# Kernel optimization log

Hardware: AMD Instinct MI355X
Metric: run time of the kernel (lower is better)

Reference implementation:

```python
import jax, jax.numpy as jnp
import numpy as np

S, B, T = 512, 256, 128


def setup_inputs() -> dict:
    key = jax.random.key(0)
    k1, k2, k3, k4, k5, k6 = jax.random.split(key, 6)
    emissions = jax.random.normal(k1, (S, B, T), dtype=jnp.float32)
    # realistic monotone mask: each sequence has a random length in [1, S]
    lengths = jax.random.randint(k2, (B,), 1, S + 1)
    mask = (jnp.arange(S)[:, None] < lengths[None, :]).astype(jnp.float32)  # [S,B]
    tags = jax.random.randint(k3, (S, B), 0, T)
    transitions = jax.random.normal(k4, (T, T), dtype=jnp.float32)
    start_transitions = jax.random.normal(k5, (T,), dtype=jnp.float32)
    stop_transitions = jax.random.normal(k6, (T,), dtype=jnp.float32)
    return {
        "emissions": emissions,
        "mask": mask,
        "tags": tags,
        "transitions": transitions,
        "start_transitions": start_transitions,
        "stop_transitions": stop_transitions,
    }


def reference(emissions, mask, tags, transitions, start_transitions, stop_transitions):
    seq_len, batch, num_tags = emissions.shape

    # ---- log-partition (forward algorithm) + viterbi score, fused scan ----
    init = start_transitions + emissions[0]  # [B,T]

    def part_step(carry, xs):
        fv, vv = carry  # forward var, viterbi var: [B,T]
        em, m = xs      # em: [B,T], m: [B]
        # scores[b, j, k] = em[b, j] + transitions[j, k]  (j=next tag, k=prev tag)
        scores = em[:, :, None] + transitions[None, :, :]          # [B,T,T]
        lse = jax.nn.logsumexp(fv[:, None, :] + scores, axis=2)     # [B,T]
        vmax = jnp.max(vv[:, None, :] + scores, axis=2)             # [B,T]
        fv = m[:, None] * lse + (1.0 - m)[:, None] * fv
        vv = m[:, None] * vmax + (1.0 - m)[:, None] * vv
        return (fv, vv), None

    (fv, vv), _ = jax.lax.scan(part_step, (init, init), (emissions[1:], mask[1:]))
    total_score = jax.nn.logsumexp(fv + stop_transitions, axis=1)   # [B]
    best_path_score = jnp.max(vv + stop_transitions, axis=1)        # [B]

    # ---- gold path score ----
    barange = jnp.arange(batch)
    tag0 = tags[0]
    rps0 = start_transitions[tag0] + emissions[0, barange, tag0] * mask[0]

    def rp_step(carry, xs):
        rps, prev = carry
        cur, em, m = xs  # cur:[B] int, em:[B,T], m:[B]
        rps = rps + transitions[prev, cur] * m
        rps = rps + jnp.take_along_axis(em, cur[:, None], axis=1)[:, 0] * m
        prev = jnp.where(m == 1.0, cur, prev)
        return (rps, prev), None

    (rps, prev), _ = jax.lax.scan(rp_step, (rps0, tag0), (tags[1:], emissions[1:], mask[1:]))
    real_path_score = rps + stop_transitions[prev]

    loss = jnp.mean(total_score - real_path_score)
    return loss, real_path_score, total_score, best_path_score
```

## Files before the change

kernel.cpp:

```cpp
#include <hip/hip_runtime.h>
#include <math.h>

#define S_LEN 512
#define BATCH 256
#define NTAG  128
#define EMSTRIDE (BATCH * NTAG)

typedef float    f32x2 __attribute__((ext_vector_type(2)));
typedef float    f32x4 __attribute__((ext_vector_type(4)));
typedef int      i32x4 __attribute__((ext_vector_type(4)));
typedef _Float16 h16x2 __attribute__((ext_vector_type(2)));

#define DPP_XOR1(x) __int_as_float(__builtin_amdgcn_mov_dpp(__float_as_int(x), 0xB1, 0xF, 0xF, false))
#define DPP_XOR2(x) __int_as_float(__builtin_amdgcn_mov_dpp(__float_as_int(x), 0x4E, 0xF, 0xF, false))

__device__ __forceinline__ int pkmax(int a, int b) {
  int r; asm("v_pk_max_f16 %0, %1, %2" : "=v"(r) : "v"(a), "v"(b)); return r;
}
__device__ __forceinline__ int pkmul(int a, int b) {
  int r; asm("v_pk_mul_f16 %0, %1, %2" : "=v"(r) : "v"(a), "v"(b)); return r;
}
__device__ __forceinline__ float dot2(int e, int w, float c) {
  return __builtin_amdgcn_fdot2(__builtin_bit_cast(h16x2, e),
                                __builtin_bit_cast(h16x2, w), c, false);
}
__device__ __forceinline__ int packh(float a, float b) {
  return __builtin_bit_cast(int, __builtin_amdgcn_cvt_pkrtz(a, b));
}
__device__ __forceinline__ f32x2 unpackh(int p) {
  h16x2 h = __builtin_bit_cast(h16x2, p);
  f32x2 r; r[0] = (float)h[0]; r[1] = (float)h[1]; return r;
}
__device__ __forceinline__ int emidx(bool isR, int len, int i) {
  int s = isR ? (len - 2 - i) : (1 + i);
  return s < 0 ? 0 : (s > S_LEN - 1 ? S_LEN - 1 : s);
}

__global__ __launch_bounds__(256, 1)
void crf_chain_kernel(const float* __restrict__ emis,
                      const float* __restrict__ mask,
                      const int* __restrict__ tags,
                      const float* __restrict__ trans,
                      const float* __restrict__ startt,
                      const float* __restrict__ stopt,
                      float* __restrict__ ws,
                      int* __restrict__ ewbuf,
                      float* __restrict__ out)
{
  const int blk = blockIdx.x;
  const int tid = threadIdx.x;

  __shared__ __align__(16) int cbuf[4][2][64];
  __shared__ float red[16];

  if (blk >= BATCH) {
    const int b = blk - BATCH;
    float part = 0.f, lenp = 0.f;
#pragma unroll
    for (int rep = 0; rep < 2; ++rep) {
      int s = tid + rep * 256;
      float m  = mask[(size_t)s * BATCH + b];
      int  cur = tags[(size_t)s * BATCH + b];
      if (s == 0) {
        part += startt[cur] + emis[(size_t)b * NTAG + cur] * m;
      } else {
        int prev = tags[(size_t)(s - 1) * BATCH + b];
        part += m * (trans[(size_t)prev * NTAG + cur] +
                     emis[((size_t)s * BATCH + b) * NTAG + cur]);
      }
      lenp += m;
    }
#pragma unroll
    for (int d = 1; d <= 32; d <<= 1) {
      part += __shfl_xor(part, d);
      lenp += __shfl_xor(lenp, d);
    }
    const int lane = tid & 63, wid = tid >> 6;
    if (lane == 0) { red[wid] = part; red[8 + wid] = lenp; }
    __syncthreads();
    if (tid == 0) {
      float rps = (red[0] + red[1]) + (red[2] + red[3]);
      float lf  = (red[8] + red[9]) + (red[10] + red[11]);
      int len = (int)(lf + 0.5f);
      int pf  = tags[(size_t)(len - 1) * BATCH + b];
      out[1 + b] = rps + stopt[pf];
    }
    return;
  }

  const int  b    = blk;
  const int  role = tid >> 6;
  const int  l    = tid & 63;
  const bool isR  = (role & 1) != 0;
  const bool isV  = (role >= 2);

  float mv = 0.f;
#pragma unroll
  for (int r = 0; r < 8; ++r) mv += mask[(size_t)(l + 64 * r) * BATCH + b];
#pragma unroll
  for (int d = 1; d <= 32; d <<= 1) mv += __shfl_xor(mv, d);
  const int len = (int)(mv + 0.5f);

  const int sm  = (len - 1) >> 1;
  const int nst = len - 1 - sm;
  const int cnt = isR ? nst : sm;

  int EA[64], EB[64];
  if (!isR) {
    const f32x4* r0 = (const f32x4*)(trans + (size_t)(2 * l) * NTAG);
    const f32x4* r1 = (const f32x4*)(trans + (size_t)(2 * l + 1) * NTAG);
#pragma unroll
    for (int mm = 0; mm < 32; ++mm) {
      f32x4 x0 = r0[mm], x1 = r1[mm];
      EA[2 * mm]     = packh(__expf(x0[0]), __expf(x0[1]));
      EA[2 * mm + 1] = packh(__expf(x0[2]), __expf(x0[3]));
      EB[2 * mm]     = packh(__expf(x1[0]), __expf(x1[1]));
      EB[2 * mm + 1] = packh(__expf(x1[2]), __expf(x1[3]));
    }
  } else {
#pragma unroll
    for (int m = 0; m < 64; ++m) {
      f32x2 p0 = *(const f32x2*)(trans + (size_t)(2 * m) * NTAG + 2 * l);
      f32x2 p1 = *(const f32x2*)(trans + (size_t)(2 * m + 1) * NTAG + 2 * l);
      EA[m] = packh(__expf(p0[0]), __expf(p1[0]));
      EB[m] = packh(__expf(p0[1]), __expf(p1[1]));
    }
  }

  const float* ebm = emis + (size_t)b * NTAG + 2 * l;
  float iA, iB;
  if (!isR) {
    iA = startt[2 * l]     + ebm[0];
    iB = startt[2 * l + 1] + ebm[1];
  } else {
    float eA = 0.f, eB = 0.f;
    if (nst > 0) {
      f32x2 e = *(const f32x2*)(ebm + (size_t)(len - 1) * EMSTRIDE);
      eA = e[0]; eB = e[1];
    }
    iA = stopt[2 * l]     + eA;
    iB = stopt[2 * l + 1] + eB;
  }
  float uA = __expf(iA), uB = __expf(iB);
  float mx0 = fmaxf(uA, uB);
  mx0 = fmaxf(mx0, DPP_XOR1(mx0));
  mx0 = fmaxf(mx0, DPP_XOR2(mx0));
  mx0 = fmaxf(mx0, __shfl_xor(mx0, 4));
  mx0 = fmaxf(mx0, __shfl_xor(mx0, 8));
  mx0 = fmaxf(mx0, __shfl_xor(mx0, 16));
  mx0 = fmaxf(mx0, __shfl_xor(mx0, 32));
  unsigned eb0 = (__float_as_uint(mx0) >> 23) & 0xFF;
  int Ew = (int)eb0 - 127;
  float sc0 = __uint_as_float((unsigned)(254 - eb0) << 23);
  cbuf[role][0][l] = packh(uA * sc0, uB * sc0);
  asm volatile("s_waitcnt lgkmcnt(0)" ::: "memory");

  f32x2 e0 = *(const f32x2*)(ebm + (size_t)emidx(isR, len, 0) * EMSTRIDE);
  f32x2 e1 = *(const f32x2*)(ebm + (size_t)emidx(isR, len, 1) * EMSTRIDE);
  f32x2 e2 = *(const f32x2*)(ebm + (size_t)emidx(isR, len, 2) * EMSTRIDE);
  f32x2 e3 = *(const f32x2*)(ebm + (size_t)emidx(isR, len, 3) * EMSTRIDE);

  int fin = cnt & 1;

#define TMAX(QQ) pkmax(pkmax(QQ[0], QQ[1]), pkmax(QQ[2], QQ[3]))

#define DQ(QQ, MB)                                                            \
      a0 = dot2(EA[(MB)+0], QQ[0], a0); b0 = dot2(EB[(MB)+0], QQ[0], b0);     \
      a1 = dot2(EA[(MB)+1], QQ[1], a1); b1 = dot2(EB[(MB)+1], QQ[1], b1);     \
      a2 = dot2(EA[(MB)+2], QQ[2], a2); b2 = dot2(EB[(MB)+2], QQ[2], b2);     \
      a3 = dot2(EA[(MB)+3], QQ[3], a3); b3 = dot2(EB[(MB)+3], QQ[3], b3);

#define VQ(QQ, MB)                                                            \
      pA0 = pkmax(pA0, pkmul(EA[(MB)+0], QQ[0]));                             \
      pB0 = pkmax(pB0, pkmul(EB[(MB)+0], QQ[0]));                             \
      pA1 = pkmax(pA1, pkmul(EA[(MB)+1], QQ[1]));                             \
      pB1 = pkmax(pB1, pkmul(EB[(MB)+1], QQ[1]));                             \
      pA2 = pkmax(pA2, pkmul(EA[(MB)+2], QQ[2]));                             \
      pB2 = pkmax(pB2, pkmul(EB[(MB)+2], QQ[2]));                             \
      pA3 = pkmax(pA3, pkmul(EA[(MB)+3], QQ[3]));                             \
      pB3 = pkmax(pB3, pkmul(EB[(MB)+3], QQ[3]));

#define STEP(U, EV)                                                           \
  {                                                                           \
    const int i_ = gb + (U);                                                  \
    if (i_ >= cnt) goto epi;                                                  \
    const i32x4* rp_ = (const i32x4*)cbuf[role][(U) & 1];                     \
    i32x4 Q0 = rp_[0],  Q1 = rp_[1],  Q2 = rp_[2],  Q3 = rp_[3];              \
    i32x4 Q4 = rp_[4],  Q5 = rp_[5],  Q6 = rp_[6],  Q7 = rp_[7];              \
    i32x4 Q8 = rp_[8],  Q9 = rp_[9],  Q10 = rp_[10], Q11 = rp_[11];           \
    i32x4 Q12 = rp_[12], Q13 = rp_[13], Q14 = rp_[14], Q15 = rp_[15];         \
    int t0 = TMAX(Q0),  t1 = TMAX(Q1),  t2 = TMAX(Q2),  t3 = TMAX(Q3);        \
    int t4 = TMAX(Q4),  t5 = TMAX(Q5),  t6 = TMAX(Q6),  t7 = TMAX(Q7);        \
    int t8 = TMAX(Q8),  t9 = TMAX(Q9),  t10 = TMAX(Q10), t11 = TMAX(Q11);     \
    int t12 = TMAX(Q12), t13 = TMAX(Q13), t14 = TMAX(Q14), t15 = TMAX(Q15);   \
    t0 = pkmax(t0, t1);   t2 = pkmax(t2, t3);                                 \
    t4 = pkmax(t4, t5);   t6 = pkmax(t6, t7);                                 \
    t8 = pkmax(t8, t9);   t10 = pkmax(t10, t11);                              \
    t12 = pkmax(t12, t13); t14 = pkmax(t14, t15);                             \
    t0 = pkmax(t0, t2); t4 = pkmax(t4, t6);                                   \
    t8 = pkmax(t8, t10); t12 = pkmax(t12, t14);                               \
    t0 = pkmax(t0, t4); t8 = pkmax(t8, t12); t0 = pkmax(t0, t8);              \
    f32x2 mh_ = unpackh(t0);                                                  \
    float mxx_ = fmaxf(mh_[0], mh_[1]);                                       \
    unsigned ebx_ = (__float_as_uint(mxx_) >> 23) & 0xFF;                     \
    float sc_ = __uint_as_float((unsigned)((isV ? 242u : 246u) - ebx_) << 23);\
    Ew += (int)ebx_ - 127 + (isV ? 12 : 8);                                   \
    const bool lastR_ = isR && (i_ == cnt - 1);                               \
    float exA_ = lastR_ ? 1.f : __expf((EV)[0]);                              \
    float exB_ = lastR_ ? 1.f : __expf((EV)[1]);                              \
    float vA_, vB_;                                                           \
    if (!isV) {                                                               \
      float a0 = 0.f, a1 = 0.f, a2 = 0.f, a3 = 0.f;                           \
      float b0 = 0.f, b1 = 0.f, b2 = 0.f, b3 = 0.f;                           \
      DQ(Q0, 0)  DQ(Q1, 4)  DQ(Q2, 8)   DQ(Q3, 12)                            \
      DQ(Q4, 16) DQ(Q5, 20) DQ(Q6, 24)  DQ(Q7, 28)                            \
      DQ(Q8, 32) DQ(Q9, 36) DQ(Q10, 40) DQ(Q11, 44)                           \
      DQ(Q12, 48) DQ(Q13, 52) DQ(Q14, 56) DQ(Q15, 60)                         \
      vA_ = (a0 + a1) + (a2 + a3);                                            \
      vB_ = (b0 + b1) + (b2 + b3);                                            \
    } else {                                                                  \
      int pA0 = 0, pA1 = 0, pA2 = 0, pA3 = 0;                                 \
      int pB0 = 0, pB1 = 0, pB2 = 0, pB3 = 0;                                 \
      VQ(Q0, 0)  VQ(Q1, 4)  VQ(Q2, 8)   VQ(Q3, 12)                            \
      VQ(Q4, 16) VQ(Q5, 20) VQ(Q6, 24)  VQ(Q7, 28)                            \
      VQ(Q8, 32) VQ(Q9, 36) VQ(Q10, 40) VQ(Q11, 44)                           \
      VQ(Q12, 48) VQ(Q13, 52) VQ(Q14, 56) VQ(Q15, 60)                         \
      int pA_ = pkmax(pkmax(pA0, pA1), pkmax(pA2, pA3));                      \
      int pB_ = pkmax(pkmax(pB0, pB1), pkmax(pB2, pB3));                      \
      f32x2 ua_ = unpackh(pA_), ub_ = unpackh(pB_);                           \
      vA_ = fmaxf(ua_[0], ua_[1]);                                            \
      vB_ = fmaxf(ub_[0], ub_[1]);                                            \
    }                                                                         \
    cbuf[role][((U) + 1) & 1][l] = packh(exA_ * vA_ * sc_, exB_ * vB_ * sc_); \
    asm volatile("s_waitcnt lgkmcnt(0)" ::: "memory");                        \
  }

  for (int gb = 0; gb < 256; gb += 4) {
    f32x2 n0 = *(const f32x2*)(ebm + (size_t)emidx(isR, len, gb + 4) * EMSTRIDE);
    f32x2 n1 = *(const f32x2*)(ebm + (size_t)emidx(isR, len, gb + 5) * EMSTRIDE);
    f32x2 n2 = *(const f32x2*)(ebm + (size_t)emidx(isR, len, gb + 6) * EMSTRIDE);
    f32x2 n3 = *(const f32x2*)(ebm + (size_t)emidx(isR, len, gb + 7) * EMSTRIDE);
    STEP(0, e0)
    STEP(1, e1)
    STEP(2, e2)
    STEP(3, e3)
    e0 = n0; e1 = n1; e2 = n2; e3 = n3;
  }

epi:
  {
    f32x2 o = unpackh(cbuf[role][fin][l]);
    *(f32x2*)(ws + (size_t)b * 512 + role * 128 + 2 * l) = o;
    if (l == 0) ewbuf[role * BATCH + b] = Ew;
  }
}

__global__ __launch_bounds__(128, 1)
void crf_combine_kernel(const float* __restrict__ ws,
                        const int* __restrict__ ewbuf,
                        float* __restrict__ out)
{
  const int b = blockIdx.x, k = threadIdx.x;
  const float* base = ws + (size_t)b * 512;
  float t1 = base[k] * base[128 + k];
  float m1 = base[256 + k] * base[384 + k];
#pragma unroll
  for (int d = 1; d <= 32; d <<= 1) {
    t1 += __shfl_xor(t1, d);
    m1 = fmaxf(m1, __shfl_xor(m1, d));
  }
  __shared__ float rs[2], rm[2];
  const int lane = k & 63, wid = k >> 6;
  if (lane == 0) { rs[wid] = t1; rm[wid] = m1; }
  __syncthreads();
  if (k == 0) {
    const double LN2 = 0.6931471805599453;
    int EtF = ewbuf[b] + ewbuf[BATCH + b];
    int EtV = ewbuf[2 * BATCH + b] + ewbuf[3 * BATCH + b];
    out[1 + BATCH + b] =
        (float)((double)EtF * LN2 + (double)__logf(rs[0] + rs[1]));
    out[1 + 2 * BATCH + b] =
        (float)((double)EtV * LN2 + (double)__logf(fmaxf(rm[0], rm[1])));
  }
}

__global__ __launch_bounds__(256, 1)
void crf_loss_kernel(float* __restrict__ out)
{
  const int tid = threadIdx.x;
  float dft = out[1 + BATCH + tid] - out[1 + tid];
#pragma unroll
  for (int d = 1; d <= 32; d <<= 1) dft += __shfl_xor(dft, d);
  __shared__ float rs[4];
  const int lane = tid & 63, wid = tid >> 6;
  if (lane == 0) rs[wid] = dft;
  __syncthreads();
  if (tid == 0)
    out[0] = ((rs[0] + rs[1]) + (rs[2] + rs[3])) * (1.0f / BATCH);
}

extern "C" void kernel_launch(void* const* d_in, const int* in_sizes, int n_in,
                              void* d_out, int out_size, void* d_ws, size_t ws_size,
                              hipStream_t stream)
{
  const float* emis   = (const float*)d_in[0];
  const float* mask   = (const float*)d_in[1];
  const int*   tags   = (const int*)d_in[2];
  const float* trans  = (const float*)d_in[3];
  const float* startt = (const float*)d_in[4];
  const float* stopt  = (const float*)d_in[5];
  float* out = (float*)d_out;

  float* wsf   = (float*)d_ws;
  int*   ewbuf = (int*)(wsf + 512 * BATCH);

  crf_chain_kernel<<<2 * BATCH, 256, 0, stream>>>(emis, mask, tags, trans,
                                                  startt, stopt, wsf, ewbuf, out);
  crf_combine_kernel<<<BATCH, 128, 0, stream>>>(wsf, ewbuf, out);
  crf_loss_kernel<<<1, 256, 0, stream>>>(out);
}
```

Before: 253.3 us.

## Replace fp16 LDS-exchange recurrence with fp32 readlane broadcast and log-domain Viterbi

```diff
diff --git a/kernel.cpp b/kernel.cpp
--- a/kernel.cpp
+++ b/kernel.cpp
@@ -6,34 +6,33 @@
 #define NTAG  128
 #define EMSTRIDE (BATCH * NTAG)
 
-typedef float    f32x2 __attribute__((ext_vector_type(2)));
-typedef float    f32x4 __attribute__((ext_vector_type(4)));
-typedef int      i32x4 __attribute__((ext_vector_type(4)));
-typedef _Float16 h16x2 __attribute__((ext_vector_type(2)));
-
-#define DPP_XOR1(x) __int_as_float(__builtin_amdgcn_mov_dpp(__float_as_int(x), 0xB1, 0xF, 0xF, false))
-#define DPP_XOR2(x) __int_as_float(__builtin_amdgcn_mov_dpp(__float_as_int(x), 0x4E, 0xF, 0xF, false))
-
-__device__ __forceinline__ int pkmax(int a, int b) {
-  int r; asm("v_pk_max_f16 %0, %1, %2" : "=v"(r) : "v"(a), "v"(b)); return r;
-}
-__device__ __forceinline__ int pkmul(int a, int b) {
-  int r; asm("v_pk_mul_f16 %0, %1, %2" : "=v"(r) : "v"(a), "v"(b)); return r;
-}
-__device__ __forceinline__ float dot2(int e, int w, float c) {
-  return __builtin_amdgcn_fdot2(__builtin_bit_cast(h16x2, e),
-                                __builtin_bit_cast(h16x2, w), c, false);
-}
-__device__ __forceinline__ int packh(float a, float b) {
-  return __builtin_bit_cast(int, __builtin_amdgcn_cvt_pkrtz(a, b));
-}
-__device__ __forceinline__ f32x2 unpackh(int p) {
-  h16x2 h = __builtin_bit_cast(h16x2, p);
-  f32x2 r; r[0] = (float)h[0]; r[1] = (float)h[1]; return r;
-}
-__device__ __forceinline__ int emidx(bool isR, int len, int i) {
+typedef float f32x2 __attribute__((ext_vector_type(2)));
+typedef float f32x4 __attribute__((ext_vector_type(4)));
+
+__device__ __forceinline__ f32x2 fma2(f32x2 a, f32x2 b, f32x2 c){
+  f32x2 r; r[0]=__builtin_fmaf(a[0],b[0],c[0]); r[1]=__builtin_fmaf(a[1],b[1],c[1]); return r;
+}
+__device__ __forceinline__ float max3f(float a, float b, float c){
+  return fmaxf(fmaxf(a,b),c);
+}
+
+#define DPPF(x, ctrl) __uint_as_float(__builtin_amdgcn_mov_dpp(__float_as_uint(x), ctrl, 0xF, 0xF, false))
+#define RL(x, m)      __uint_as_float(__builtin_amdgcn_readlane(__float_as_uint(x), m))
+
+__device__ __forceinline__ float wavemax_pos(float x) {
+  x = fmaxf(x, DPPF(x, 0xB1));
+  x = fmaxf(x, DPPF(x, 0x4E));
+  x = fmaxf(x, DPPF(x, 0x124));
+  x = fmaxf(x, DPPF(x, 0x128));
+  x = fmaxf(x, DPPF(x, 0x142));
+  x = fmaxf(x, DPPF(x, 0x143));
+  return RL(x, 63);
+}
+
+__device__ __forceinline__ int emt(bool isR, int len, int i) {
   int s = isR ? (len - 2 - i) : (1 + i);
-  return s < 0 ? 0 : (s > S_LEN - 1 ? S_LEN - 1 : s);
+  s = s < 0 ? 0 : s;
+  return s > S_LEN - 1 ? S_LEN - 1 : s;
 }
 
 __global__ __launch_bounds__(256, 1)
@@ -50,7 +49,6 @@
   const int blk = blockIdx.x;
   const int tid = threadIdx.x;
 
-  __shared__ __align__(16) int cbuf[4][2][64];
   __shared__ float red[16];
 
   if (blk >= BATCH) {
@@ -105,153 +103,122 @@
   const int nst = len - 1 - sm;
   const int cnt = isR ? nst : sm;
 
-  int EA[64], EB[64];
+  f32x2 M0[64], M1[64];
   if (!isR) {
-    const f32x4* r0 = (const f32x4*)(trans + (size_t)(2 * l) * NTAG);
-    const f32x4* r1 = (const f32x4*)(trans + (size_t)(2 * l + 1) * NTAG);
-#pragma unroll
-    for (int mm = 0; mm < 32; ++mm) {
-      f32x4 x0 = r0[mm], x1 = r1[mm];
-      EA[2 * mm]     = packh(__expf(x0[0]), __expf(x0[1]));
-      EA[2 * mm + 1] = packh(__expf(x0[2]), __expf(x0[3]));
-      EB[2 * mm]     = packh(__expf(x1[0]), __expf(x1[1]));
-      EB[2 * mm + 1] = packh(__expf(x1[2]), __expf(x1[3]));
+    const float* r0 = trans + (size_t)(2 * l) * NTAG;
+    const float* r1 = r0 + NTAG;
+#pragma unroll
+    for (int m = 0; m < 64; ++m) {
+      M0[m] = *(const f32x2*)(r0 + 2 * m);
+      M1[m] = *(const f32x2*)(r1 + 2 * m);
     }
   } else {
+    const float* tc = trans + 2 * l;
 #pragma unroll
     for (int m = 0; m < 64; ++m) {
-      f32x2 p0 = *(const f32x2*)(trans + (size_t)(2 * m) * NTAG + 2 * l);
-      f32x2 p1 = *(const f32x2*)(trans + (size_t)(2 * m + 1) * NTAG + 2 * l);
-      EA[m] = packh(__expf(p0[0]), __expf(p1[0]));
-      EB[m] = packh(__expf(p0[1]), __expf(p1[1]));
+      f32x2 p0 = *(const f32x2*)(tc + (size_t)(2 * m) * NTAG);
+      f32x2 p1 = *(const f32x2*)(tc + (size_t)(2 * m + 1) * NTAG);
+      f32x2 a; a[0] = p0[0]; a[1] = p1[0];
+      f32x2 c; c[0] = p0[1]; c[1] = p1[1];
+      M0[m] = a; M1[m] = c;
+    }
+  }
+  if (!isV) {
+#pragma unroll
+    for (int m = 0; m < 64; ++m) {
+      M0[m][0] = __expf(M0[m][0]); M0[m][1] = __expf(M0[m][1]);
+      M1[m][0] = __expf(M1[m][0]); M1[m][1] = __expf(M1[m][1]);
     }
   }
 
   const float* ebm = emis + (size_t)b * NTAG + 2 * l;
-  float iA, iB;
-  if (!isR) {
-    iA = startt[2 * l]     + ebm[0];
-    iB = startt[2 * l + 1] + ebm[1];
-  } else {
-    float eA = 0.f, eB = 0.f;
-    if (nst > 0) {
-      f32x2 e = *(const f32x2*)(ebm + (size_t)(len - 1) * EMSTRIDE);
-      eA = e[0]; eB = e[1];
-    }
-    iA = stopt[2 * l]     + eA;
-    iB = stopt[2 * l + 1] + eB;
-  }
-  float uA = __expf(iA), uB = __expf(iB);
-  float mx0 = fmaxf(uA, uB);
-  mx0 = fmaxf(mx0, DPP_XOR1(mx0));
-  mx0 = fmaxf(mx0, DPP_XOR2(mx0));
-  mx0 = fmaxf(mx0, __shfl_xor(mx0, 4));
-  mx0 = fmaxf(mx0, __shfl_xor(mx0, 8));
-  mx0 = fmaxf(mx0, __shfl_xor(mx0, 16));
-  mx0 = fmaxf(mx0, __shfl_xor(mx0, 32));
-  unsigned eb0 = (__float_as_uint(mx0) >> 23) & 0xFF;
-  int Ew = (int)eb0 - 127;
-  float sc0 = __uint_as_float((unsigned)(254 - eb0) << 23);
-  cbuf[role][0][l] = packh(uA * sc0, uB * sc0);
-  asm volatile("s_waitcnt lgkmcnt(0)" ::: "memory");
-
-  f32x2 e0 = *(const f32x2*)(ebm + (size_t)emidx(isR, len, 0) * EMSTRIDE);
-  f32x2 e1 = *(const f32x2*)(ebm + (size_t)emidx(isR, len, 1) * EMSTRIDE);
-  f32x2 e2 = *(const f32x2*)(ebm + (size_t)emidx(isR, len, 2) * EMSTRIDE);
-  f32x2 e3 = *(const f32x2*)(ebm + (size_t)emidx(isR, len, 3) * EMSTRIDE);
-
-  int fin = cnt & 1;
-
-#define TMAX(QQ) pkmax(pkmax(QQ[0], QQ[1]), pkmax(QQ[2], QQ[3]))
-
-#define DQ(QQ, MB)                                                            \
-      a0 = dot2(EA[(MB)+0], QQ[0], a0); b0 = dot2(EB[(MB)+0], QQ[0], b0);     \
-      a1 = dot2(EA[(MB)+1], QQ[1], a1); b1 = dot2(EB[(MB)+1], QQ[1], b1);     \
-      a2 = dot2(EA[(MB)+2], QQ[2], a2); b2 = dot2(EB[(MB)+2], QQ[2], b2);     \
-      a3 = dot2(EA[(MB)+3], QQ[3], a3); b3 = dot2(EB[(MB)+3], QQ[3], b3);
-
-#define VQ(QQ, MB)                                                            \
-      pA0 = pkmax(pA0, pkmul(EA[(MB)+0], QQ[0]));                             \
-      pB0 = pkmax(pB0, pkmul(EB[(MB)+0], QQ[0]));                             \
-      pA1 = pkmax(pA1, pkmul(EA[(MB)+1], QQ[1]));                             \
-      pB1 = pkmax(pB1, pkmul(EB[(MB)+1], QQ[1]));                             \
-      pA2 = pkmax(pA2, pkmul(EA[(MB)+2], QQ[2]));                             \
-      pB2 = pkmax(pB2, pkmul(EB[(MB)+2], QQ[2]));                             \
-      pA3 = pkmax(pA3, pkmul(EA[(MB)+3], QQ[3]));                             \
-      pB3 = pkmax(pB3, pkmul(EB[(MB)+3], QQ[3]));
-
-#define STEP(U, EV)                                                           \
+  float w0, w1;
+  {
+    f32x2 s0;
+    if (!isR) {
+      f32x2 st = *(const f32x2*)(startt + 2 * l);
+      s0 = st + *(const f32x2*)ebm;
+    } else {
+      f32x2 st = *(const f32x2*)(stopt + 2 * l);
+      f32x2 eL = {0.f, 0.f};
+      if (nst > 0) eL = *(const f32x2*)(ebm + (size_t)(len - 1) * EMSTRIDE);
+      s0 = st + eL;
+    }
+    w0 = isV ? s0[0] : __expf(s0[0]);
+    w1 = isV ? s0[1] : __expf(s0[1]);
+  }
+  int Ew = 0;
+
+  f32x2 e0 = *(const f32x2*)(ebm + (size_t)emt(isR, len, 0) * EMSTRIDE);
+  f32x2 e1 = *(const f32x2*)(ebm + (size_t)emt(isR, len, 1) * EMSTRIDE);
+  f32x2 e2 = *(const f32x2*)(ebm + (size_t)emt(isR, len, 2) * EMSTRIDE);
+  f32x2 e3 = *(const f32x2*)(ebm + (size_t)emt(isR, len, 3) * EMSTRIDE);
+
+#define STEP(U, EV, RN)                                                       \
   {                                                                           \
     const int i_ = gb + (U);                                                  \
     if (i_ >= cnt) goto epi;                                                  \
-    const i32x4* rp_ = (const i32x4*)cbuf[role][(U) & 1];                     \
-    i32x4 Q0 = rp_[0],  Q1 = rp_[1],  Q2 = rp_[2],  Q3 = rp_[3];              \
-    i32x4 Q4 = rp_[4],  Q5 = rp_[5],  Q6 = rp_[6],  Q7 = rp_[7];              \
-    i32x4 Q8 = rp_[8],  Q9 = rp_[9],  Q10 = rp_[10], Q11 = rp_[11];           \
-    i32x4 Q12 = rp_[12], Q13 = rp_[13], Q14 = rp_[14], Q15 = rp_[15];         \
-    int t0 = TMAX(Q0),  t1 = TMAX(Q1),  t2 = TMAX(Q2),  t3 = TMAX(Q3);        \
-    int t4 = TMAX(Q4),  t5 = TMAX(Q5),  t6 = TMAX(Q6),  t7 = TMAX(Q7);        \
-    int t8 = TMAX(Q8),  t9 = TMAX(Q9),  t10 = TMAX(Q10), t11 = TMAX(Q11);     \
-    int t12 = TMAX(Q12), t13 = TMAX(Q13), t14 = TMAX(Q14), t15 = TMAX(Q15);   \
-    t0 = pkmax(t0, t1);   t2 = pkmax(t2, t3);                                 \
-    t4 = pkmax(t4, t5);   t6 = pkmax(t6, t7);                                 \
-    t8 = pkmax(t8, t9);   t10 = pkmax(t10, t11);                              \
-    t12 = pkmax(t12, t13); t14 = pkmax(t14, t15);                             \
-    t0 = pkmax(t0, t2); t4 = pkmax(t4, t6);                                   \
-    t8 = pkmax(t8, t10); t12 = pkmax(t12, t14);                               \
-    t0 = pkmax(t0, t4); t8 = pkmax(t8, t12); t0 = pkmax(t0, t8);              \
-    f32x2 mh_ = unpackh(t0);                                                  \
-    float mxx_ = fmaxf(mh_[0], mh_[1]);                                       \
-    unsigned ebx_ = (__float_as_uint(mxx_) >> 23) & 0xFF;                     \
-    float sc_ = __uint_as_float((unsigned)((isV ? 242u : 246u) - ebx_) << 23);\
-    Ew += (int)ebx_ - 127 + (isV ? 12 : 8);                                   \
     const bool lastR_ = isR && (i_ == cnt - 1);                               \
-    float exA_ = lastR_ ? 1.f : __expf((EV)[0]);                              \
-    float exB_ = lastR_ ? 1.f : __expf((EV)[1]);                              \
-    float vA_, vB_;                                                           \
     if (!isV) {                                                               \
-      float a0 = 0.f, a1 = 0.f, a2 = 0.f, a3 = 0.f;                           \
-      float b0 = 0.f, b1 = 0.f, b2 = 0.f, b3 = 0.f;                           \
-      DQ(Q0, 0)  DQ(Q1, 4)  DQ(Q2, 8)   DQ(Q3, 12)                            \
-      DQ(Q4, 16) DQ(Q5, 20) DQ(Q6, 24)  DQ(Q7, 28)                            \
-      DQ(Q8, 32) DQ(Q9, 36) DQ(Q10, 40) DQ(Q11, 44)                           \
-      DQ(Q12, 48) DQ(Q13, 52) DQ(Q14, 56) DQ(Q15, 60)                         \
-      vA_ = (a0 + a1) + (a2 + a3);                                            \
-      vB_ = (b0 + b1) + (b2 + b3);                                            \
+      f32x2 aA0 = {0.f,0.f}, aA1 = {0.f,0.f};                                 \
+      f32x2 aB0 = {0.f,0.f}, aB1 = {0.f,0.f};                                 \
+      _Pragma("unroll")                                                       \
+      for (int m = 0; m < 64; ++m) {                                          \
+        f32x2 sp; sp[0] = RL(w0, m); sp[1] = RL(w1, m);                       \
+        if (m & 1) { aA1 = fma2(M0[m], sp, aA1); aB1 = fma2(M1[m], sp, aB1); }\
+        else       { aA0 = fma2(M0[m], sp, aA0); aB0 = fma2(M1[m], sp, aB0); }\
+      }                                                                       \
+      f32x2 aA = aA0 + aA1, aB = aB0 + aB1;                                   \
+      float sA = aA[0] + aA[1], sB = aB[0] + aB[1];                           \
+      float ex0 = 1.f, ex1 = 1.f;                                             \
+      if (!lastR_) { ex0 = __expf((EV)[0]); ex1 = __expf((EV)[1]); }          \
+      if (RN) {                                                               \
+        float mx_ = wavemax_pos(fmaxf(w0, w1));                               \
+        int ew_ = (int)((__float_as_uint(mx_) >> 23) & 0xFF) - 126;           \
+        Ew += ew_;                                                            \
+        float sc_ = __uint_as_float((unsigned)(127 - ew_) << 23);             \
+        w0 = ex0 * sA * sc_; w1 = ex1 * sB * sc_;                             \
+      } else {                                                                \
+        w0 = ex0 * sA; w1 = ex1 * sB;                                         \
+      }                                                                       \
     } else {                                                                  \
-      int pA0 = 0, pA1 = 0, pA2 = 0, pA3 = 0;                                 \
-      int pB0 = 0, pB1 = 0, pB2 = 0, pB3 = 0;                                 \
-      VQ(Q0, 0)  VQ(Q1, 4)  VQ(Q2, 8)   VQ(Q3, 12)                            \
-      VQ(Q4, 16) VQ(Q5, 20) VQ(Q6, 24)  VQ(Q7, 28)                            \
-      VQ(Q8, 32) VQ(Q9, 36) VQ(Q10, 40) VQ(Q11, 44)                           \
-      VQ(Q12, 48) VQ(Q13, 52) VQ(Q14, 56) VQ(Q15, 60)                         \
-      int pA_ = pkmax(pkmax(pA0, pA1), pkmax(pA2, pA3));                      \
-      int pB_ = pkmax(pkmax(pB0, pB1), pkmax(pB2, pB3));                      \
-      f32x2 ua_ = unpackh(pA_), ub_ = unpackh(pB_);                           \
-      vA_ = fmaxf(ua_[0], ua_[1]);                                            \
-      vB_ = fmaxf(ub_[0], ub_[1]);                                            \
+      float mA0 = -3.0e38f, mA1 = -3.0e38f;                                   \
+      float mB0 = -3.0e38f, mB1 = -3.0e38f;                                   \
+      _Pragma("unroll")                                                       \
+      for (int m = 0; m < 64; ++m) {                                          \
+        f32x2 sp; sp[0] = RL(w0, m); sp[1] = RL(w1, m);                       \
+        f32x2 t0 = sp + M0[m];                                                \
+        f32x2 t1 = sp + M1[m];                                                \
+        if (m & 1) { mA1 = max3f(mA1, t0[0], t0[1]);                          \
+                     mB1 = max3f(mB1, t1[0], t1[1]); }                        \
+        else       { mA0 = max3f(mA0, t0[0], t0[1]);                          \
+                     mB0 = max3f(mB0, t1[0], t1[1]); }                        \
+      }                                                                       \
+      float sA = fmaxf(mA0, mA1), sB = fmaxf(mB0, mB1);                       \
+      w0 = lastR_ ? sA : sA + (EV)[0];                                        \
+      w1 = lastR_ ? sB : sB + (EV)[1];                                        \
     }                                                                         \
-    cbuf[role][((U) + 1) & 1][l] = packh(exA_ * vA_ * sc_, exB_ * vB_ * sc_); \
-    asm volatile("s_waitcnt lgkmcnt(0)" ::: "memory");                        \
   }
 
   for (int gb = 0; gb < 256; gb += 4) {
-    f32x2 n0 = *(const f32x2*)(ebm + (size_t)emidx(isR, len, gb + 4) * EMSTRIDE);
-    f32x2 n1 = *(const f32x2*)(ebm + (size_t)emidx(isR, len, gb + 5) * EMSTRIDE);
-    f32x2 n2 = *(const f32x2*)(ebm + (size_t)emidx(isR, len, gb + 6) * EMSTRIDE);
-    f32x2 n3 = *(const f32x2*)(ebm + (size_t)emidx(isR, len, gb + 7) * EMSTRIDE);
-    STEP(0, e0)
-    STEP(1, e1)
-    STEP(2, e2)
-    STEP(3, e3)
+    f32x2 n0 = *(const f32x2*)(ebm + (size_t)emt(isR, len, gb + 4) * EMSTRIDE);
+    f32x2 n1 = *(const f32x2*)(ebm + (size_t)emt(isR, len, gb + 5) * EMSTRIDE);
+    f32x2 n2 = *(const f32x2*)(ebm + (size_t)emt(isR, len, gb + 6) * EMSTRIDE);
+    f32x2 n3 = *(const f32x2*)(ebm + (size_t)emt(isR, len, gb + 7) * EMSTRIDE);
+
+    STEP(0, e0, 0)
+    STEP(1, e1, 0)
+    STEP(2, e2, 0)
+    STEP(3, e3, 1)
+
     e0 = n0; e1 = n1; e2 = n2; e3 = n3;
   }
 
 epi:
   {
-    f32x2 o = unpackh(cbuf[role][fin][l]);
+    f32x2 o; o[0] = w0; o[1] = w1;
     *(f32x2*)(ws + (size_t)b * 512 + role * 128 + 2 * l) = o;
-    if (l == 0) ewbuf[role * BATCH + b] = Ew;
+    if (l == 0 && !isV) ewbuf[(role & 1) * BATCH + b] = Ew;
   }
 }
 
@@ -263,7 +230,7 @@
   const int b = blockIdx.x, k = threadIdx.x;
   const float* base = ws + (size_t)b * 512;
   float t1 = base[k] * base[128 + k];
-  float m1 = base[256 + k] * base[384 + k];
+  float m1 = base[256 + k] + base[384 + k];
 #pragma unroll
   for (int d = 1; d <= 32; d <<= 1) {
     t1 += __shfl_xor(t1, d);
@@ -275,12 +242,9 @@
   __syncthreads();
   if (k == 0) {
     const double LN2 = 0.6931471805599453;
-    int EtF = ewbuf[b] + ewbuf[BATCH + b];
-    int EtV = ewbuf[2 * BATCH + b] + ewbuf[3 * BATCH + b];
-    out[1 + BATCH + b] =
-        (float)((double)EtF * LN2 + (double)__logf(rs[0] + rs[1]));
-    out[1 + 2 * BATCH + b] =
-        (float)((double)EtV * LN2 + (double)__logf(fmaxf(rm[0], rm[1])));
+    int Et = ewbuf[b] + ewbuf[BATCH + b];
+    out[1 + BATCH + b]     = (float)((double)Et * LN2 + (double)__logf(rs[0] + rs[1]));
+    out[1 + 2 * BATCH + b] = fmaxf(rm[0], rm[1]);
   }
 }
 
```

Measured after the change: 305.0 us. +20.4%, slower.
